# Performance work log

Hardware: AMD Instinct MI355X
Metric: run time of the kernel (lower is better)

The kernel has to match this reference:

```python
import jax, jax.numpy as jnp
import numpy as np


def _chamfer(array1, array2):
    # array1: [B, N, 3], array2: [B, M, 3]
    sq1 = jnp.sum(array1 * array1, axis=-1)            # [B, N]
    sq2 = jnp.sum(array2 * array2, axis=-1)            # [B, M]
    inner = jnp.einsum('bnd,bmd->bnm', array1, array2)  # [B, N, M]
    d = sq1[:, :, None] + sq2[:, None, :] - 2.0 * inner  # [B, N, M]
    d = jnp.maximum(d, 0.0)  # clamp tiny negatives from cancellation
    dist1 = jnp.min(d, axis=2)  # [B, N] nearest in array2 for each pt in array1
    dist2 = jnp.min(d, axis=1)  # [B, M] nearest in array1 for each pt in array2
    return dist1, dist2


def setup_inputs() -> dict:
    key = jax.random.key(0)
    k1, k2 = jax.random.split(key)
    B, N, M = 8, 4096, 4096
    array1 = jax.random.normal(k1, (B, N, 3), dtype=jnp.float32)
    array2 = jax.random.normal(k2, (B, M, 3), dtype=jnp.float32)
    return {"array1": array1, "array2": array2}


def reference(array1, array2):
    dist1, dist2 = _chamfer(array1, array2)
    return jnp.mean(dist1) + jnp.mean(dist2)
```

## Files before the change

kernel.cpp:

```cpp
#include <hip/hip_runtime.h>
#include <math.h>

#define BATCH   8
#define NPTS    4096
#define TOTAL   (BATCH * NPTS)
#define THREADS 256
#define P       8
#define TILE    (THREADS * P)
#define TILES   (TOTAL / TILE)
#define CHUNKS  32
#define CHUNK   (NPTS / CHUNKS)
#define NBLOCK  (2 * TILES * CHUNKS)


__global__ __launch_bounds__(THREADS)
void chamfer_kernel(const float* __restrict__ a1, const float* __restrict__ a2,
                    unsigned* __restrict__ dist) {
    const int bid   = blockIdx.x;
    const int dir   = bid >> 9;
    const int r     = bid & 511;
    const int tile  = r >> 5;
    const int chunk = r & 31;
    const int batch = tile >> 1;

    const float* __restrict__ sraw = dir ? a2 : a1;
    const float* __restrict__ qraw = dir ? a1 : a2;

    __shared__ float4 lq[CHUNK];
    if (threadIdx.x < CHUNK) {
        const int p = batch * NPTS + chunk * CHUNK + threadIdx.x;
        const float* __restrict__ g = qraw + 3 * p;
        float x = g[0], y = g[1], z = g[2];
        lq[threadIdx.x] = make_float4(-2.0f * x, -2.0f * y, -2.0f * z,
                                      fmaf(x, x, fmaf(y, y, z * z)));
    }

    float xs[P], ys[P], zs[P], sq[P];
    #pragma unroll
    for (int k = 0; k < P; k++) {
        int si = tile * TILE + k * THREADS + threadIdx.x;
        float x = sraw[3 * si + 0];
        float y = sraw[3 * si + 1];
        float z = sraw[3 * si + 2];
        xs[k] = x;
        ys[k] = y;
        zs[k] = z;
        sq[k] = fmaf(x, x, fmaf(y, y, z * z));
    }
    __syncthreads();

    float acc[P];
    #pragma unroll
    for (int k = 0; k < P; k++) acc[k] = __builtin_inff();

    #pragma unroll 2
    for (int j = 0; j < CHUNK; j += 2) {
        float4 q0 = lq[j];
        float4 q1 = lq[j + 1];
        #pragma unroll
        for (int k = 0; k < P; k++) {
            float d0 = fmaf(q0.x, xs[k], fmaf(q0.y, ys[k], fmaf(q0.z, zs[k], q0.w)));
            float d1 = fmaf(q1.x, xs[k], fmaf(q1.y, ys[k], fmaf(q1.z, zs[k], q1.w)));
            acc[k] = fminf(fminf(d0, d1), acc[k]);
        }
    }

    #pragma unroll
    for (int k = 0; k < P; k++) {
        int si = tile * TILE + k * THREADS + threadIdx.x;
        float dmin = fmaxf(acc[k] + sq[k], 0.0f);
        atomicMin(dist + dir * TOTAL + si, __float_as_uint(dmin));
    }
}

__global__ __launch_bounds__(1024)
void reduce_kernel(const float* __restrict__ dist, float* __restrict__ out) {
    const float4* __restrict__ dv = (const float4*)dist;
    float s = 0.0f;
    #pragma unroll
    for (int i = 0; i < (2 * TOTAL / 4) / 1024; i++) {
        float4 v = dv[i * 1024 + threadIdx.x];
        s += (v.x + v.y) + (v.z + v.w);
    }
    #pragma unroll
    for (int off = 32; off > 0; off >>= 1) s += __shfl_down(s, off, 64);
    __shared__ float wsum[16];
    if ((threadIdx.x & 63) == 0) wsum[threadIdx.x >> 6] = s;
    __syncthreads();
    if (threadIdx.x < 16) {
        float v = wsum[threadIdx.x];
        #pragma unroll
        for (int off = 8; off > 0; off >>= 1) v += __shfl_down(v, off, 16);
        if (threadIdx.x == 0) out[0] = v * (1.0f / (float)TOTAL);
    }
}

extern "C" void kernel_launch(void* const* d_in, const int* in_sizes, int n_in,
                              void* d_out, int out_size, void* d_ws, size_t ws_size,
                              hipStream_t stream) {
    const float* a1 = (const float*)d_in[0];
    const float* a2 = (const float*)d_in[1];
    float* out = (float*)d_out;

    unsigned* dist = (unsigned*)d_ws;

    chamfer_kernel<<<NBLOCK, THREADS, 0, stream>>>(a1, a2, dist);
    reduce_kernel<<<1, 1024, 0, stream>>>((const float*)dist, out);
}
```

Measured before the change: 78.42 us.

## Compute chamfer distances with bf16 split-precision MFMA matrix tiles

Recasts the pairwise squared-distance computation as a K=32 bf16 matrix multiply. Coordinates and squared norms are split into high and low bf16 parts so the MFMA output directly gives the full distance, and a pack kernel builds the fragments beforehand. Row minima are reduced in registers and column minima go to 8 replicated atomicMin buffers to cut contention, which are merged in a multi-block reduce. This trades exactness for matrix-core throughput, so the split-bf16 terms may leave small accuracy error, and the extra pack and reduce launches add overhead.

```diff
diff --git a/kernel.cpp b/kernel.cpp
--- a/kernel.cpp
+++ b/kernel.cpp
@@ -4,95 +4,160 @@
 #define BATCH   8
 #define NPTS    4096
 #define TOTAL   (BATCH * NPTS)
-#define THREADS 256
-#define P       8
-#define TILE    (THREADS * P)
-#define TILES   (TOTAL / TILE)
-#define CHUNKS  32
-#define CHUNK   (NPTS / CHUNKS)
-#define NBLOCK  (2 * TILES * CHUNKS)
+#define NTILES  (TOTAL / 16)
+#define MSPLIT  4
+#define ITERS   (256 / MSPLIT)
+#define NWAVES  (BATCH * 128 * MSPLIT)
+#define NREP    8
+
+typedef __attribute__((ext_vector_type(8))) short bfrag;
+typedef __attribute__((ext_vector_type(4))) float ffrag;
+
+__device__ __forceinline__ unsigned short bf16_rne(float f) {
+    unsigned u = __float_as_uint(f);
+    return (unsigned short)((u + 0x7FFFu + ((u >> 16) & 1u)) >> 16);
+}
+__device__ __forceinline__ float bf16f(unsigned short h) {
+    return __uint_as_float(((unsigned)h) << 16);
+}
 
 
-__global__ __launch_bounds__(THREADS)
-void chamfer_kernel(const float* __restrict__ a1, const float* __restrict__ a2,
-                    unsigned* __restrict__ dist) {
-    const int bid   = blockIdx.x;
-    const int dir   = bid >> 9;
-    const int r     = bid & 511;
-    const int tile  = r >> 5;
-    const int chunk = r & 31;
-    const int batch = tile >> 1;
+__global__ __launch_bounds__(256)
+void pack_kernel(const float* __restrict__ a1, const float* __restrict__ a2,
+                 uint4* __restrict__ Abuf, uint4* __restrict__ Bbuf,
+                 float* __restrict__ out) {
+    const int w    = blockIdx.x * 4 + (threadIdx.x >> 6);
+    const int lane = threadIdx.x & 63;
+    const int koct = lane >> 4;
+    const int idx  = lane & 15;
+    const bool isA = (w < NTILES);
+    const int tile = isA ? w : (w - NTILES);
+    const float* __restrict__ src = isA ? a1 : a2;
+    const int p = tile * 16 + idx;
+    float x = src[3 * p + 0], y = src[3 * p + 1], z = src[3 * p + 2];
+    float s = fmaf(x, x, fmaf(y, y, z * z));
+    const unsigned short ONE = 0x3F80;
+    unsigned short v[8] = {0, 0, 0, 0, 0, 0, 0, 0};
+    if (isA) {
+        if (koct == 0) {
+            unsigned short xh = bf16_rne(x), xl = bf16_rne(x - bf16f(xh));
+            unsigned short yh = bf16_rne(y), yl = bf16_rne(y - bf16f(yh));
+            unsigned short zh = bf16_rne(z);
+            v[0]=xh; v[1]=xh; v[2]=xl; v[3]=yh; v[4]=yh; v[5]=yl; v[6]=zh; v[7]=zh;
+        } else if (koct == 1) {
+            unsigned short zh = bf16_rne(z), zl = bf16_rne(z - bf16f(zh));
+            unsigned short sh = bf16_rne(s), sl = bf16_rne(s - bf16f(sh));
+            v[0]=zl; v[1]=ONE; v[2]=ONE; v[3]=sh; v[4]=sl;
+        }
+    } else {
+        float X = -2.f * x, Y = -2.f * y, Z = -2.f * z;
+        if (koct == 0) {
+            unsigned short Xh = bf16_rne(X), Xl = bf16_rne(X - bf16f(Xh));
+            unsigned short Yh = bf16_rne(Y), Yl = bf16_rne(Y - bf16f(Yh));
+            unsigned short Zh = bf16_rne(Z), Zl = bf16_rne(Z - bf16f(Zh));
+            v[0]=Xh; v[1]=Xl; v[2]=Xh; v[3]=Yh; v[4]=Yl; v[5]=Yh; v[6]=Zh; v[7]=Zl;
+        } else if (koct == 1) {
+            unsigned short Zh = bf16_rne(Z);
+            unsigned short Wh = bf16_rne(s), Wl = bf16_rne(s - bf16f(Wh));
+            v[0]=Zh; v[1]=Wh; v[2]=Wl; v[3]=ONE; v[4]=ONE;
+        }
+    }
+    uint4 pk;
+    pk.x = (unsigned)v[0] | ((unsigned)v[1] << 16);
+    pk.y = (unsigned)v[2] | ((unsigned)v[3] << 16);
+    pk.z = (unsigned)v[4] | ((unsigned)v[5] << 16);
+    pk.w = (unsigned)v[6] | ((unsigned)v[7] << 16);
+    (isA ? Abuf : Bbuf)[(size_t)tile * 64 + lane] = pk;
+    if (blockIdx.x == 0 && threadIdx.x == 0) out[0] = 0.0f;
+}
 
-    const float* __restrict__ sraw = dir ? a2 : a1;
-    const float* __restrict__ qraw = dir ? a1 : a2;
+__global__ __launch_bounds__(256)
+void chamfer_mfma_kernel(const uint4* __restrict__ Abuf_, const uint4* __restrict__ Bbuf_,
+                         unsigned* __restrict__ dist1, unsigned* __restrict__ dist2) {
+    const int w    = blockIdx.x * 4 + (threadIdx.x >> 6);
+    const int lane = threadIdx.x & 63;
+    const int batch  = w >> 9;
+    const int rem    = w & 511;
+    const int msplit = rem >> 7;
+    const int nwave  = rem & 127;
 
-    __shared__ float4 lq[CHUNK];
-    if (threadIdx.x < CHUNK) {
-        const int p = batch * NPTS + chunk * CHUNK + threadIdx.x;
-        const float* __restrict__ g = qraw + 3 * p;
-        float x = g[0], y = g[1], z = g[2];
-        lq[threadIdx.x] = make_float4(-2.0f * x, -2.0f * y, -2.0f * z,
-                                      fmaf(x, x, fmaf(y, y, z * z)));
-    }
+    const int ntile0 = batch * 256 + nwave * 2;
+    const int mt0    = batch * 256 + msplit * ITERS;
 
-    float xs[P], ys[P], zs[P], sq[P];
+    const bfrag* __restrict__ Af = (const bfrag*)Abuf_;
+    const bfrag* __restrict__ Bf = (const bfrag*)Bbuf_;
+    bfrag a0 = Af[(size_t)ntile0 * 64 + lane];
+    bfrag a1 = Af[(size_t)(ntile0 + 1) * 64 + lane];
+    const bfrag* __restrict__ Bp = Bf + (size_t)mt0 * 64 + lane;
+
+    unsigned* __restrict__ d2 = dist2 + (size_t)(nwave & (NREP - 1)) * TOTAL;
+
+    const ffrag zero = {0.f, 0.f, 0.f, 0.f};
+    float racc[8];
     #pragma unroll
-    for (int k = 0; k < P; k++) {
-        int si = tile * TILE + k * THREADS + threadIdx.x;
-        float x = sraw[3 * si + 0];
-        float y = sraw[3 * si + 1];
-        float z = sraw[3 * si + 2];
-        xs[k] = x;
-        ys[k] = y;
-        zs[k] = z;
-        sq[k] = fmaf(x, x, fmaf(y, y, z * z));
-    }
-    __syncthreads();
+    for (int q = 0; q < 8; q++) racc[q] = __builtin_inff();
 
-    float acc[P];
-    #pragma unroll
-    for (int k = 0; k < P; k++) acc[k] = __builtin_inff();
-
-    #pragma unroll 2
-    for (int j = 0; j < CHUNK; j += 2) {
-        float4 q0 = lq[j];
-        float4 q1 = lq[j + 1];
+    bfrag bcur = Bp[0];
+    for (int it = 0; it < ITERS; it++) {
+        bfrag bnxt = Bp[(size_t)(it + 1) * 64];
+        ffrag c0 = __builtin_amdgcn_mfma_f32_16x16x32_bf16(a0, bcur, zero, 0, 0, 0);
+        ffrag c1 = __builtin_amdgcn_mfma_f32_16x16x32_bf16(a1, bcur, zero, 0, 0, 0);
         #pragma unroll
-        for (int k = 0; k < P; k++) {
-            float d0 = fmaf(q0.x, xs[k], fmaf(q0.y, ys[k], fmaf(q0.z, zs[k], q0.w)));
-            float d1 = fmaf(q1.x, xs[k], fmaf(q1.y, ys[k], fmaf(q1.z, zs[k], q1.w)));
-            acc[k] = fminf(fminf(d0, d1), acc[k]);
-        }
+        for (int q = 0; q < 4; q++) racc[q]     = fminf(racc[q],     c0[q]);
+        #pragma unroll
+        for (int q = 0; q < 4; q++) racc[4 + q] = fminf(racc[4 + q], c1[q]);
+        float cm = fminf(fminf(fminf(c0[0], c0[1]), fminf(c0[2], c0[3])),
+                         fminf(fminf(c1[0], c1[1]), fminf(c1[2], c1[3])));
+        cm = fminf(cm, __shfl_xor(cm, 16));
+        cm = fminf(cm, __shfl_xor(cm, 32));
+        cm = fmaxf(cm, 0.f);
+        if (lane < 16)
+            atomicMin(d2 + (size_t)(mt0 + it) * 16 + lane, __float_as_uint(cm));
+        bcur = bnxt;
     }
 
     #pragma unroll
-    for (int k = 0; k < P; k++) {
-        int si = tile * TILE + k * THREADS + threadIdx.x;
-        float dmin = fmaxf(acc[k] + sq[k], 0.0f);
-        atomicMin(dist + dir * TOTAL + si, __float_as_uint(dmin));
+    for (int q = 0; q < 8; q++) {
+        float v = racc[q];
+        v = fminf(v, __shfl_xor(v, 1));
+        v = fminf(v, __shfl_xor(v, 2));
+        v = fminf(v, __shfl_xor(v, 4));
+        v = fminf(v, __shfl_xor(v, 8));
+        racc[q] = fmaxf(v, 0.f);
+    }
+    if ((lane & 15) == 0) {
+        const int quad = lane >> 4;
+        unsigned* __restrict__ b0 = dist1 + ntile0 * 16 + quad * 4;
+        #pragma unroll
+        for (int rI = 0; rI < 4; rI++) atomicMin(b0 + rI, __float_as_uint(racc[rI]));
+        unsigned* __restrict__ b1 = dist1 + (ntile0 + 1) * 16 + quad * 4;
+        #pragma unroll
+        for (int rI = 0; rI < 4; rI++) atomicMin(b1 + rI, __float_as_uint(racc[4 + rI]));
     }
 }
 
-__global__ __launch_bounds__(1024)
-void reduce_kernel(const float* __restrict__ dist, float* __restrict__ out) {
-    const float4* __restrict__ dv = (const float4*)dist;
-    float s = 0.0f;
+__global__ __launch_bounds__(256)
+void reduce_kernel(const unsigned* __restrict__ dist1,
+                   const unsigned* __restrict__ dist2, float* __restrict__ out) {
+    const int t = blockIdx.x * 256 + threadIdx.x;
+    float s = 0.f;
     #pragma unroll
-    for (int i = 0; i < (2 * TOTAL / 4) / 1024; i++) {
-        float4 v = dv[i * 1024 + threadIdx.x];
-        s += (v.x + v.y) + (v.z + v.w);
+    for (int part = 0; part < 2; part++) {
+        const int i = part * 16384 + t;
+        s += __uint_as_float(dist1[i]);
+        float mn = __uint_as_float(dist2[i]);
+        #pragma unroll
+        for (int rp = 1; rp < NREP; rp++)
+            mn = fminf(mn, __uint_as_float(dist2[(size_t)rp * TOTAL + i]));
+        s += mn;
     }
     #pragma unroll
     for (int off = 32; off > 0; off >>= 1) s += __shfl_down(s, off, 64);
-    __shared__ float wsum[16];
+    __shared__ float wsum[4];
     if ((threadIdx.x & 63) == 0) wsum[threadIdx.x >> 6] = s;
     __syncthreads();
-    if (threadIdx.x < 16) {
-        float v = wsum[threadIdx.x];
-        #pragma unroll
-        for (int off = 8; off > 0; off >>= 1) v += __shfl_down(v, off, 16);
-        if (threadIdx.x == 0) out[0] = v * (1.0f / (float)TOTAL);
-    }
+    if (threadIdx.x == 0)
+        atomicAdd(out, (wsum[0] + wsum[1] + wsum[2] + wsum[3]) * (1.0f / (float)TOTAL));
 }
 
 extern "C" void kernel_launch(void* const* d_in, const int* in_sizes, int n_in,
@@ -102,8 +167,13 @@
     const float* a2 = (const float*)d_in[1];
     float* out = (float*)d_out;
 
-    unsigned* dist = (unsigned*)d_ws;
+    char* ws = (char*)d_ws;
+    uint4*    Abuf  = (uint4*)ws;
+    uint4*    Bbuf  = (uint4*)(ws + (size_t)NTILES * 1024);
+    unsigned* dist1 = (unsigned*)(ws + (size_t)2 * NTILES * 1024 + 1024);
+    unsigned* dist2 = dist1 + TOTAL;
 
-    chamfer_kernel<<<NBLOCK, THREADS, 0, stream>>>(a1, a2, dist);
-    reduce_kernel<<<1, 1024, 0, stream>>>((const float*)dist, out);
+    pack_kernel<<<(2 * NTILES) / 4, 256, 0, stream>>>(a1, a2, Abuf, Bbuf, out);
+    chamfer_mfma_kernel<<<NWAVES / 4, 256, 0, stream>>>(Abuf, Bbuf, dist1, dist2);
+    reduce_kernel<<<64, 256, 0, stream>>>(dist1, dist2, out);
 }
```

Result: slower. 94.94 us (+21.1%).
